# Kernel optimization log

Hardware: AMD Instinct MI355X
Metric: run time of the kernel (lower is better)

The kernel has to match this reference:

```python
import jax, jax.numpy as jnp
import numpy as np

N, L, S, H, D = 4, 2048, 2048, 8, 64

def setup_inputs() -> dict:
    key = jax.random.key(0)
    kq, kk, kv = jax.random.split(key, 3)
    queries = jax.random.normal(kq, (N, L, H, D), dtype=jnp.float32)
    keys = jax.random.normal(kk, (N, S, H, D), dtype=jnp.float32)
    values = jax.random.normal(kv, (N, S, H, D), dtype=jnp.float32)
    q_mask = jnp.ones((N, L), dtype=bool)
    kv_mask = jnp.ones((N, S), dtype=bool)
    return {"queries": queries, "keys": keys, "values": values,
            "q_mask": q_mask, "kv_mask": kv_mask}

def reference(queries, keys, values, q_mask, kv_mask):
    # QK: [N, L, S, H]
    QK = jnp.einsum('nlhd,nshd->nlsh', queries, keys)
    if kv_mask is not None:
        mask = q_mask[:, :, None, None] & kv_mask[:, None, :, None]  # [N,L,S,1]
        QK = jnp.where(mask, QK, -jnp.inf)
    softmax_temp = 1.0 / (queries.shape[3] ** 0.5)
    A = jax.nn.softmax(softmax_temp * QK, axis=2)  # softmax over S
    queried_values = jnp.einsum('nlsh,nshd->nlhd', A, values)
    return queried_values
```

## Files before the change

### kernel.cpp

```cpp
#include <hip/hip_runtime.h>
#include <hip/hip_bf16.h>
#include <math.h>

typedef __bf16 bf16_t;
typedef __bf16 bf16x2 __attribute__((ext_vector_type(2)));
typedef __bf16 bf16x4 __attribute__((ext_vector_type(4)));
typedef __bf16 bf16x8 __attribute__((ext_vector_type(8)));
typedef float floatx4 __attribute__((ext_vector_type(4)));

constexpr int N_ = 4, L_ = 2048, S_ = 2048, H_ = 8, D_ = 64;

__device__ __forceinline__ void async_load16(const void* g, void* l) {
  __builtin_amdgcn_global_load_lds(
      (const __attribute__((address_space(1))) void*)g,
      (__attribute__((address_space(3))) void*)l, 16, 0, 0);
}

__global__ __launch_bounds__(256)
void prep(const float* __restrict__ Kg, const float* __restrict__ Vg,
          bf16_t* __restrict__ Kb, bf16_t* __restrict__ Vtb) {
  __shared__ bf16x2 pr_sh[64 * 33];
  const int tid = threadIdx.x;
  const int nh = blockIdx.y, s0 = blockIdx.x * 64;
  const int n = nh >> 3, h = nh & 7;
  {
    const int srow = tid >> 2, d0 = (tid & 3) * 16;
    const float* kp = Kg + (((size_t)n * S_ + s0 + srow) * H_ + h) * D_ + d0;
    float4 x0 = ((const float4*)kp)[0], x1 = ((const float4*)kp)[1];
    float4 x2 = ((const float4*)kp)[2], x3 = ((const float4*)kp)[3];
    bf16x8 f0, f1;
    f0[0] = (bf16_t)x0.x; f0[1] = (bf16_t)x0.y; f0[2] = (bf16_t)x0.z; f0[3] = (bf16_t)x0.w;
    f0[4] = (bf16_t)x1.x; f0[5] = (bf16_t)x1.y; f0[6] = (bf16_t)x1.z; f0[7] = (bf16_t)x1.w;
    f1[0] = (bf16_t)x2.x; f1[1] = (bf16_t)x2.y; f1[2] = (bf16_t)x2.z; f1[3] = (bf16_t)x2.w;
    f1[4] = (bf16_t)x3.x; f1[5] = (bf16_t)x3.y; f1[6] = (bf16_t)x3.z; f1[7] = (bf16_t)x3.w;
    *(bf16x8*)&Kb[((size_t)nh * S_ + s0 + srow) * D_ + d0] = f0;
    *(bf16x8*)&Kb[((size_t)nh * S_ + s0 + srow) * D_ + d0 + 8] = f1;
  }
  {
    const int s2 = tid >> 3;
    const int dg = (tid & 7) * 8;
    const float* vp0 = Vg + (((size_t)n * S_ + s0 + 2 * s2) * H_ + h) * D_ + dg;
    const float* vp1 = vp0 + (size_t)H_ * D_;
    float4 a0 = ((const float4*)vp0)[0], a1 = ((const float4*)vp0)[1];
    float4 b0 = ((const float4*)vp1)[0], b1 = ((const float4*)vp1)[1];
    float r0[8] = { a0.x, a0.y, a0.z, a0.w, a1.x, a1.y, a1.z, a1.w };
    float r1[8] = { b0.x, b0.y, b0.z, b0.w, b1.x, b1.y, b1.z, b1.w };
#pragma unroll
    for (int j = 0; j < 8; ++j) {
      bf16x2 pr; pr[0] = (bf16_t)r0[j]; pr[1] = (bf16_t)r1[j];
      pr_sh[(dg + j) * 33 + s2] = pr;
    }
  }
  __syncthreads();
  {
    const int dr = tid >> 2, sq = tid & 3;
    bf16x8 o0, o1;
#pragma unroll
    for (int p = 0; p < 4; ++p) {
      bf16x2 v = pr_sh[dr * 33 + sq * 8 + p];
      o0[2 * p] = v[0]; o0[2 * p + 1] = v[1];
    }
#pragma unroll
    for (int p = 0; p < 4; ++p) {
      bf16x2 v = pr_sh[dr * 33 + sq * 8 + 4 + p];
      o1[2 * p] = v[0]; o1[2 * p + 1] = v[1];
    }
    bf16_t* op = &Vtb[((size_t)nh * D_ + dr) * S_ + s0 + sq * 16];
    *(bf16x8*)op = o0;
    *(bf16x8*)(op + 8) = o1;
  }
}

__global__ __launch_bounds__(256, 2)
void fattn(const float* __restrict__ Qg, const bf16_t* __restrict__ Kb,
           const bf16_t* __restrict__ Vtb, float* __restrict__ Og) {
  __shared__ __align__(16) char smem[4 * 12288];

  const int tid  = threadIdx.x;
  const int wave = tid >> 6;
  const int lane = tid & 63;
  const int quad = lane >> 4;
  const int l16  = lane & 15;
  char* wbase = smem + wave * 12288;
  bf16_t* kbuf = (bf16_t*)(wbase);
  bf16_t* vbuf = (bf16_t*)(wbase + 4096);
  bf16_t* pw   = (bf16_t*)(wbase + 8192);

  const int lb = blockIdx.x;
  const int nh = (lb & 7) * 4 + ((lb >> 3) & 3);
  const int qb = lb >> 5;
  const int n  = nh >> 3;
  const int h  = nh & 7;
  const int l0 = qb * 64;

  const float qs = 0.125f * 1.44269504088896340736f;
  bf16x8 qf[4][2];
#pragma unroll
  for (int nbq = 0; nbq < 4; ++nbq) {
    const int q = l0 + nbq * 16 + l16;
    const float* qp = Qg + (((size_t)n * L_ + q) * H_ + h) * D_;
#pragma unroll
    for (int kc = 0; kc < 2; ++kc) {
      const float* p = qp + kc * 32 + quad * 8;
      float4 a = ((const float4*)p)[0];
      float4 b = ((const float4*)p)[1];
      bf16x8 f;
      f[0] = (bf16_t)(a.x * qs); f[1] = (bf16_t)(a.y * qs);
      f[2] = (bf16_t)(a.z * qs); f[3] = (bf16_t)(a.w * qs);
      f[4] = (bf16_t)(b.x * qs); f[5] = (bf16_t)(b.y * qs);
      f[6] = (bf16_t)(b.z * qs); f[7] = (bf16_t)(b.w * qs);
      qf[nbq][kc] = f;
    }
  }

  floatx4 oacc[4][4];
#pragma unroll
  for (int a = 0; a < 4; ++a)
#pragma unroll
    for (int b = 0; b < 4; ++b) oacc[a][b] = (floatx4){0.f, 0.f, 0.f, 0.f};
  float lsum_p[4] = {0.f, 0.f, 0.f, 0.f};

  const bf16_t* kbase = Kb + (size_t)nh * S_ * D_;
  const bf16_t* vbase = Vtb + (size_t)nh * D_ * S_;

  const int krr  = lane >> 3;
  const int kcol = ((lane & 7) ^ ((lane >> 3) & 7)) * 8;
  const int vrr  = lane >> 2;
  const int vcol = ((lane & 3) ^ ((lane >> 3) & 3)) * 8;

  {
    const int s0w = wave * 32;
#pragma unroll
    for (int i = 0; i < 4; ++i)
      async_load16(kbase + (size_t)(s0w + i * 8 + krr) * 64 + kcol,
                   (char*)kbuf + i * 1024);
#pragma unroll
    for (int i = 0; i < 4; ++i)
      async_load16(vbase + (size_t)(i * 16 + vrr) * S_ + s0w + vcol,
                   (char*)vbuf + i * 1024);
  }

  bf16x8 zf;
#pragma unroll
  for (int i = 0; i < 8; ++i) zf[i] = (bf16_t)0.0f;
  bf16x8 pa[4]  = { zf, zf, zf, zf };
  bf16x8 vbp[4] = { zf, zf, zf, zf };

  for (int t = 0; t < 16; ++t) {
    asm volatile("s_waitcnt vmcnt(0)" ::: "memory");

    bf16x8 ka[2][2];
#pragma unroll
    for (int mb = 0; mb < 2; ++mb)
#pragma unroll
      for (int kc = 0; kc < 2; ++kc)
        ka[mb][kc] = *(const bf16x8*)
            &kbuf[(mb * 16 + l16) * 64 + (((kc * 4 + quad) ^ (l16 & 7)) * 8)];

    bf16x8 vb[4];
#pragma unroll
    for (int nbd = 0; nbd < 4; ++nbd) {
      const int row = nbd * 16 + l16;
      vb[nbd] = *(const bf16x8*)
          &vbuf[row * 32 + ((quad ^ ((row >> 1) & 3)) * 8)];
    }

    asm volatile("s_waitcnt lgkmcnt(0)" ::: "memory");

    if (t < 15) {
      const int s0n = wave * 32 + (t + 1) * 128;
#pragma unroll
      for (int i = 0; i < 4; ++i)
        async_load16(kbase + (size_t)(s0n + i * 8 + krr) * 64 + kcol,
                     (char*)kbuf + i * 1024);
#pragma unroll
      for (int i = 0; i < 4; ++i)
        async_load16(vbase + (size_t)(i * 16 + vrr) * S_ + s0n + vcol,
                     (char*)vbuf + i * 1024);
    }

#pragma unroll
    for (int mbq = 0; mbq < 4; ++mbq)
#pragma unroll
      for (int nbd = 0; nbd < 4; ++nbd)
        oacc[mbq][nbd] = __builtin_amdgcn_mfma_f32_16x16x32_bf16(
            pa[mbq], vbp[nbd], oacc[mbq][nbd], 0, 0, 0);

#pragma unroll
    for (int nbq = 0; nbq < 4; ++nbq) {
#pragma unroll
      for (int mb = 0; mb < 2; ++mb) {
        floatx4 acc = (floatx4){0.f, 0.f, 0.f, 0.f};
        acc = __builtin_amdgcn_mfma_f32_16x16x32_bf16(ka[mb][0], qf[nbq][0], acc, 0, 0, 0);
        acc = __builtin_amdgcn_mfma_f32_16x16x32_bf16(ka[mb][1], qf[nbq][1], acc, 0, 0, 0);
        float e0 = __builtin_amdgcn_exp2f(acc[0]);
        float e1 = __builtin_amdgcn_exp2f(acc[1]);
        float e2 = __builtin_amdgcn_exp2f(acc[2]);
        float e3 = __builtin_amdgcn_exp2f(acc[3]);
        lsum_p[nbq] += (e0 + e1) + (e2 + e3);
        bf16x4 pk;
        pk[0] = (bf16_t)e0; pk[1] = (bf16_t)e1;
        pk[2] = (bf16_t)e2; pk[3] = (bf16_t)e3;
        const int q = nbq * 16 + l16;
        const int c = mb * 2 + (quad >> 1);
        *(bf16x4*)&pw[q * 32 + ((c ^ ((q >> 1) & 3)) * 8) + (quad & 1) * 4] = pk;
      }
    }

#pragma unroll
    for (int mbq = 0; mbq < 4; ++mbq) {
      const int q = mbq * 16 + l16;
      pa[mbq] = *(const bf16x8*)&pw[q * 32 + ((quad ^ ((q >> 1) & 3)) * 8)];
    }
#pragma unroll
    for (int nbd = 0; nbd < 4; ++nbd) vbp[nbd] = vb[nbd];
  }

#pragma unroll
  for (int mbq = 0; mbq < 4; ++mbq)
#pragma unroll
    for (int nbd = 0; nbd < 4; ++nbd)
      oacc[mbq][nbd] = __builtin_amdgcn_mfma_f32_16x16x32_bf16(
          pa[mbq], vbp[nbd], oacc[mbq][nbd], 0, 0, 0);

#pragma unroll
  for (int nbq = 0; nbq < 4; ++nbq) {
    lsum_p[nbq] += __shfl_xor(lsum_p[nbq], 16, 64);
    lsum_p[nbq] += __shfl_xor(lsum_p[nbq], 32, 64);
  }
  float* ls_w = (float*)(wbase + 4352);
  if (quad == 0) {
#pragma unroll
    for (int nbq = 0; nbq < 4; ++nbq)
      ls_w[nbq * 16 + l16] = lsum_p[nbq];
  }
  __syncthreads();

  for (int tc = 0; tc < 4; ++tc) {
    float* red_w = (float*)wbase;
#pragma unroll
    for (int nbd = 0; nbd < 4; ++nbd)
#pragma unroll
      for (int r = 0; r < 4; ++r)
        red_w[(quad * 4 + r) * 68 + nbd * 16 + l16] = oacc[tc][nbd][r];
    __syncthreads();
    if (wave == tc) {
#pragma unroll
      for (int p = 0; p < 4; ++p) {
        const int q16 = p * 4 + quad;
        float lt = 0.f;
        float sx = 0.f, sy = 0.f, sz = 0.f, sw = 0.f;
#pragma unroll
        for (int w = 0; w < 4; ++w) {
          lt += ((const float*)(smem + w * 12288 + 4352))[tc * 16 + q16];
          const float* rp = (const float*)(smem + w * 12288);
          float4 v = *(const float4*)&rp[q16 * 68 + l16 * 4];
          sx += v.x; sy += v.y; sz += v.z; sw += v.w;
        }
        const float li = 1.f / lt;
        float4 o; o.x = sx * li; o.y = sy * li; o.z = sz * li; o.w = sw * li;
        *(float4*)&Og[(((size_t)n * L_ + l0 + tc * 16 + q16) * H_ + h) * D_ +
                      l16 * 4] = o;
      }
    }
    if (tc < 3) __syncthreads();
  }
}

extern "C" void kernel_launch(void* const* d_in, const int* in_sizes, int n_in,
                              void* d_out, int out_size, void* d_ws, size_t ws_size,
                              hipStream_t stream) {
  const float* Q = (const float*)d_in[0];
  const float* K = (const float*)d_in[1];
  const float* V = (const float*)d_in[2];
  float* O = (float*)d_out;

  bf16_t* Kb  = (bf16_t*)d_ws;
  bf16_t* Vtb = Kb + (size_t)N_ * H_ * S_ * D_;

  prep<<<dim3(S_ / 64, N_ * H_), 256, 0, stream>>>(K, V, Kb, Vtb);
  fattn<<<dim3(32 * 32, 1), 256, 0, stream>>>(Q, Kb, Vtb, O);
}
```

Before: 143.7 us.

## Split waves 2x2 over queries and keys and keep P in registers

Reorganizes the attention kernel so each wave handles 32 queries over half of the key range, rather than all 64 queries over an interleaved quarter. P is repacked in registers with permlane swaps instead of a round trip through LDS, which removes the software-pipelined pa/vbp carry, and MFMA sections get s_setprio hints. The smaller per-wave state and LDS footprint allow launch bounds of 4 blocks per SM, and the final reduction now sums only two partials. The cost is twice as many K/V tile loads per query, since each K/V tile now serves 32 queries, and a serial dependency from QK through exp to PV inside each iteration.

```diff
diff --git a/kernel.cpp b/kernel.cpp
--- a/kernel.cpp
+++ b/kernel.cpp
@@ -71,20 +71,21 @@
   }
 }
 
-__global__ __launch_bounds__(256, 2)
+__global__ __launch_bounds__(256, 4)
 void fattn(const float* __restrict__ Qg, const bf16_t* __restrict__ Kb,
            const bf16_t* __restrict__ Vtb, float* __restrict__ Og) {
-  __shared__ __align__(16) char smem[4 * 12288];
+  __shared__ __align__(16) char smem[35328];
 
   const int tid  = threadIdx.x;
   const int wave = tid >> 6;
   const int lane = tid & 63;
   const int quad = lane >> 4;
   const int l16  = lane & 15;
-  char* wbase = smem + wave * 12288;
+  const int qh   = wave >> 1;
+  const int sh   = wave & 1;
+  char* wbase = smem + wave * 8192;
   bf16_t* kbuf = (bf16_t*)(wbase);
   bf16_t* vbuf = (bf16_t*)(wbase + 4096);
-  bf16_t* pw   = (bf16_t*)(wbase + 8192);
 
   const int lb = blockIdx.x;
   const int nh = (lb & 7) * 4 + ((lb >> 3) & 3);
@@ -94,10 +95,10 @@
   const int l0 = qb * 64;
 
   const float qs = 0.125f * 1.44269504088896340736f;
-  bf16x8 qf[4][2];
-#pragma unroll
-  for (int nbq = 0; nbq < 4; ++nbq) {
-    const int q = l0 + nbq * 16 + l16;
+  bf16x8 qf[2][2];
+#pragma unroll
+  for (int nbq = 0; nbq < 2; ++nbq) {
+    const int q = l0 + qh * 32 + nbq * 16 + l16;
     const float* qp = Qg + (((size_t)n * L_ + q) * H_ + h) * D_;
 #pragma unroll
     for (int kc = 0; kc < 2; ++kc) {
@@ -113,12 +114,12 @@
     }
   }
 
-  floatx4 oacc[4][4];
-#pragma unroll
-  for (int a = 0; a < 4; ++a)
+  floatx4 oacc[2][4];
+#pragma unroll
+  for (int a = 0; a < 2; ++a)
 #pragma unroll
     for (int b = 0; b < 4; ++b) oacc[a][b] = (floatx4){0.f, 0.f, 0.f, 0.f};
-  float lsum_p[4] = {0.f, 0.f, 0.f, 0.f};
+  float lsum_p[2] = {0.f, 0.f};
 
   const bf16_t* kbase = Kb + (size_t)nh * S_ * D_;
   const bf16_t* vbase = Vtb + (size_t)nh * D_ * S_;
@@ -128,8 +129,10 @@
   const int vrr  = lane >> 2;
   const int vcol = ((lane & 3) ^ ((lane >> 3) & 3)) * 8;
 
-  {
-    const int s0w = wave * 32;
+  const int sbase = sh * 1024;
+
+  {
+    const int s0w = sbase;
 #pragma unroll
     for (int i = 0; i < 4; ++i)
       async_load16(kbase + (size_t)(s0w + i * 8 + krr) * 64 + kcol,
@@ -140,13 +143,7 @@
                    (char*)vbuf + i * 1024);
   }
 
-  bf16x8 zf;
-#pragma unroll
-  for (int i = 0; i < 8; ++i) zf[i] = (bf16_t)0.0f;
-  bf16x8 pa[4]  = { zf, zf, zf, zf };
-  bf16x8 vbp[4] = { zf, zf, zf, zf };
-
-  for (int t = 0; t < 16; ++t) {
+  for (int t = 0; t < 32; ++t) {
     asm volatile("s_waitcnt vmcnt(0)" ::: "memory");
 
     bf16x8 ka[2][2];
@@ -167,8 +164,8 @@
 
     asm volatile("s_waitcnt lgkmcnt(0)" ::: "memory");
 
-    if (t < 15) {
-      const int s0n = wave * 32 + (t + 1) * 128;
+    if (t < 31) {
+      const int s0n = sbase + (t + 1) * 32;
 #pragma unroll
       for (int i = 0; i < 4; ++i)
         async_load16(kbase + (size_t)(s0n + i * 8 + krr) * 64 + kcol,
@@ -179,91 +176,95 @@
                      (char*)vbuf + i * 1024);
     }
 
-#pragma unroll
-    for (int mbq = 0; mbq < 4; ++mbq)
-#pragma unroll
-      for (int nbd = 0; nbd < 4; ++nbd)
-        oacc[mbq][nbd] = __builtin_amdgcn_mfma_f32_16x16x32_bf16(
-            pa[mbq], vbp[nbd], oacc[mbq][nbd], 0, 0, 0);
-
-#pragma unroll
-    for (int nbq = 0; nbq < 4; ++nbq) {
+    floatx4 sacc[2][2];
+    __builtin_amdgcn_s_setprio(1);
+#pragma unroll
+    for (int nbq = 0; nbq < 2; ++nbq)
 #pragma unroll
       for (int mb = 0; mb < 2; ++mb) {
         floatx4 acc = (floatx4){0.f, 0.f, 0.f, 0.f};
         acc = __builtin_amdgcn_mfma_f32_16x16x32_bf16(ka[mb][0], qf[nbq][0], acc, 0, 0, 0);
         acc = __builtin_amdgcn_mfma_f32_16x16x32_bf16(ka[mb][1], qf[nbq][1], acc, 0, 0, 0);
-        float e0 = __builtin_amdgcn_exp2f(acc[0]);
-        float e1 = __builtin_amdgcn_exp2f(acc[1]);
-        float e2 = __builtin_amdgcn_exp2f(acc[2]);
-        float e3 = __builtin_amdgcn_exp2f(acc[3]);
-        lsum_p[nbq] += (e0 + e1) + (e2 + e3);
-        bf16x4 pk;
-        pk[0] = (bf16_t)e0; pk[1] = (bf16_t)e1;
-        pk[2] = (bf16_t)e2; pk[3] = (bf16_t)e3;
-        const int q = nbq * 16 + l16;
-        const int c = mb * 2 + (quad >> 1);
-        *(bf16x4*)&pw[q * 32 + ((c ^ ((q >> 1) & 3)) * 8) + (quad & 1) * 4] = pk;
+        sacc[nbq][mb] = acc;
       }
-    }
-
-#pragma unroll
-    for (int mbq = 0; mbq < 4; ++mbq) {
-      const int q = mbq * 16 + l16;
-      pa[mbq] = *(const bf16x8*)&pw[q * 32 + ((quad ^ ((q >> 1) & 3)) * 8)];
-    }
-#pragma unroll
-    for (int nbd = 0; nbd < 4; ++nbd) vbp[nbd] = vb[nbd];
-  }
-
-#pragma unroll
-  for (int mbq = 0; mbq < 4; ++mbq)
-#pragma unroll
-    for (int nbd = 0; nbd < 4; ++nbd)
-      oacc[mbq][nbd] = __builtin_amdgcn_mfma_f32_16x16x32_bf16(
-          pa[mbq], vbp[nbd], oacc[mbq][nbd], 0, 0, 0);
-
-#pragma unroll
-  for (int nbq = 0; nbq < 4; ++nbq) {
+    __builtin_amdgcn_s_setprio(0);
+
+    bf16x8 pa[2];
+#pragma unroll
+    for (int nbq = 0; nbq < 2; ++nbq) {
+      float e00 = __builtin_amdgcn_exp2f(sacc[nbq][0][0]);
+      float e01 = __builtin_amdgcn_exp2f(sacc[nbq][0][1]);
+      float e02 = __builtin_amdgcn_exp2f(sacc[nbq][0][2]);
+      float e03 = __builtin_amdgcn_exp2f(sacc[nbq][0][3]);
+      float e10 = __builtin_amdgcn_exp2f(sacc[nbq][1][0]);
+      float e11 = __builtin_amdgcn_exp2f(sacc[nbq][1][1]);
+      float e12 = __builtin_amdgcn_exp2f(sacc[nbq][1][2]);
+      float e13 = __builtin_amdgcn_exp2f(sacc[nbq][1][3]);
+      lsum_p[nbq] += ((e00 + e01) + (e02 + e03)) + ((e10 + e11) + (e12 + e13));
+      unsigned int w00, w01, w10, w11;
+      asm("v_cvt_pk_bf16_f32 %0, %1, %2" : "=v"(w00) : "v"(e00), "v"(e01));
+      asm("v_cvt_pk_bf16_f32 %0, %1, %2" : "=v"(w01) : "v"(e02), "v"(e03));
+      asm("v_cvt_pk_bf16_f32 %0, %1, %2" : "=v"(w10) : "v"(e10), "v"(e11));
+      asm("v_cvt_pk_bf16_f32 %0, %1, %2" : "=v"(w11) : "v"(e12), "v"(e13));
+      auto sa = __builtin_amdgcn_permlane32_swap(w00, w10, false, false);
+      auto xa = __builtin_amdgcn_permlane16_swap(sa[0], sa[1], false, false);
+      auto sb = __builtin_amdgcn_permlane32_swap(w01, w11, false, false);
+      auto xb = __builtin_amdgcn_permlane16_swap(sb[0], sb[1], false, false);
+      union { unsigned int u[4]; bf16x8 v; } pk_;
+      pk_.u[0] = xa[0]; pk_.u[1] = xb[0]; pk_.u[2] = xa[1]; pk_.u[3] = xb[1];
+      pa[nbq] = pk_.v;
+    }
+
+    __builtin_amdgcn_s_setprio(1);
+#pragma unroll
+    for (int mbq = 0; mbq < 2; ++mbq)
+#pragma unroll
+      for (int nbd = 0; nbd < 4; ++nbd)
+        oacc[mbq][nbd] = __builtin_amdgcn_mfma_f32_16x16x32_bf16(
+            pa[mbq], vb[nbd], oacc[mbq][nbd], 0, 0, 0);
+    __builtin_amdgcn_s_setprio(0);
+  }
+
+#pragma unroll
+  for (int nbq = 0; nbq < 2; ++nbq) {
     lsum_p[nbq] += __shfl_xor(lsum_p[nbq], 16, 64);
     lsum_p[nbq] += __shfl_xor(lsum_p[nbq], 32, 64);
   }
-  float* ls_w = (float*)(wbase + 4352);
+
+  __syncthreads();
+  float* red_w = (float*)smem + wave * 2176;
+#pragma unroll
+  for (int mbq = 0; mbq < 2; ++mbq)
+#pragma unroll
+    for (int nbd = 0; nbd < 4; ++nbd)
+#pragma unroll
+      for (int r = 0; r < 4; ++r)
+        red_w[(mbq * 16 + quad * 4 + r) * 68 + nbd * 16 + l16] =
+            oacc[mbq][nbd][r];
+  float* ls = (float*)(smem + 34816);
   if (quad == 0) {
 #pragma unroll
-    for (int nbq = 0; nbq < 4; ++nbq)
-      ls_w[nbq * 16 + l16] = lsum_p[nbq];
+    for (int nbq = 0; nbq < 2; ++nbq)
+      ls[wave * 32 + nbq * 16 + l16] = lsum_p[nbq];
   }
   __syncthreads();
 
-  for (int tc = 0; tc < 4; ++tc) {
-    float* red_w = (float*)wbase;
-#pragma unroll
-    for (int nbd = 0; nbd < 4; ++nbd)
-#pragma unroll
-      for (int r = 0; r < 4; ++r)
-        red_w[(quad * 4 + r) * 68 + nbd * 16 + l16] = oacc[tc][nbd][r];
-    __syncthreads();
-    if (wave == tc) {
-#pragma unroll
-      for (int p = 0; p < 4; ++p) {
-        const int q16 = p * 4 + quad;
-        float lt = 0.f;
-        float sx = 0.f, sy = 0.f, sz = 0.f, sw = 0.f;
-#pragma unroll
-        for (int w = 0; w < 4; ++w) {
-          lt += ((const float*)(smem + w * 12288 + 4352))[tc * 16 + q16];
-          const float* rp = (const float*)(smem + w * 12288);
-          float4 v = *(const float4*)&rp[q16 * 68 + l16 * 4];
-          sx += v.x; sy += v.y; sz += v.z; sw += v.w;
-        }
-        const float li = 1.f / lt;
-        float4 o; o.x = sx * li; o.y = sy * li; o.z = sz * li; o.w = sw * li;
-        *(float4*)&Og[(((size_t)n * L_ + l0 + tc * 16 + q16) * H_ + h) * D_ +
-                      l16 * 4] = o;
-      }
-    }
-    if (tc < 3) __syncthreads();
+  const float* redA = (float*)smem + (2 * (wave >> 1)) * 2176;
+  const float* redB = redA + 2176;
+  const float* lsA  = ls + (wave >> 1) * 64;
+#pragma unroll
+  for (int p = 0; p < 4; ++p) {
+    const int lr  = p * 4 + quad;
+    const int q32 = (wave & 1) * 16 + lr;
+    const int qo  = (wave >> 1) * 32 + q32;
+    const float lt = lsA[q32] + lsA[32 + q32];
+    float4 a = *(const float4*)&redA[q32 * 68 + l16 * 4];
+    float4 b = *(const float4*)&redB[q32 * 68 + l16 * 4];
+    const float li = 1.f / lt;
+    float4 o;
+    o.x = (a.x + b.x) * li; o.y = (a.y + b.y) * li;
+    o.z = (a.z + b.z) * li; o.w = (a.w + b.w) * li;
+    *(float4*)&Og[(((size_t)n * L_ + l0 + qo) * H_ + h) * D_ + l16 * 4] = o;
   }
 }
 
```

Measured after the change: 148.2 us. +3.2%, slower.
